# Optimization experiments

Measured on AMD Instinct MI355X. Metric: run time of the kernel, lower is better.

Reference implementation:

```python
import jax, jax.numpy as jnp
import numpy as np

NUM_EXPERTS = 8


def setup_inputs() -> dict:
    key = jax.random.key(0)
    k1, k2, k3, k4, k5 = jax.random.split(key, 5)
    T, D, DFF, E, K = 2048, 2048, 1024, NUM_EXPERTS, 2
    hidden_states = jax.random.normal(k1, (T, D), dtype=jnp.float32)
    w1 = jax.random.normal(k2, (E, 2 * DFF, D), dtype=jnp.float32) * 0.02
    w2 = jax.random.normal(k3, (E, D, DFF), dtype=jnp.float32) * 0.02
    topk_weights = jax.random.uniform(k4, (T, K), dtype=jnp.float32)
    topk_weights = topk_weights / jnp.sum(topk_weights, axis=-1, keepdims=True)
    topk_ids = jax.random.randint(k5, (T, K), 0, E, dtype=jnp.int32)
    return {"hidden_states": hidden_states, "w1": w1, "w2": w2,
            "topk_weights": topk_weights, "topk_ids": topk_ids}


def _expert_fn(x, w1_e, w2_e):
    # x: [T, D], w1_e: [2*DFF, D], w2_e: [D, DFF]
    gu = x @ w1_e.T                      # [T, 2*DFF]
    dff = w2_e.shape[1]
    gate, up = gu[:, :dff], gu[:, dff:]
    h = jax.nn.silu(gate) * up           # SiLU-and-mul activation
    return h @ w2_e.T                    # [T, D]


def reference(hidden_states, w1, w2, topk_weights, topk_ids):
    T = hidden_states.shape[0]
    E = w1.shape[0]
    # route[t, e] = sum_k topk_weights[t,k] * (topk_ids[t,k] == e)
    route = jnp.zeros((T, E), dtype=hidden_states.dtype)
    route = route.at[jnp.arange(T)[:, None], topk_ids].add(topk_weights)
    # per-expert dense GEMMs (E is small and fixed), then weighted combine
    outs = jax.vmap(lambda w1_e, w2_e: _expert_fn(hidden_states, w1_e, w2_e))(w1, w2)  # [E, T, D]
    return jnp.einsum('te,etd->td', route, outs)
```

## Files before the change

### kernel.cpp

```cpp
#include <hip/hip_runtime.h>
#include <hip/hip_bf16.h>
#include <stdint.h>

typedef __attribute__((ext_vector_type(4))) float f32x4;
typedef __attribute__((ext_vector_type(8))) short bf16x8;
typedef unsigned short u16;

#define T_TOK   2048
#define D_DIM   2048
#define DFF_DIM 1024
#define NEXP    8
#define TOPK    2
#define NROWS   (T_TOK * TOPK)
#define BM      128
#define BK      64
#define MAX_MB  40
#define GRID_G  (16 * MAX_MB)

#define XB_OFF    65536
#define XB_BYTES  ((size_t)T_TOK * D_DIM * 2)
#define H_OFF     (XB_OFF + XB_BYTES)
#define H_BYTES   ((size_t)NROWS * DFF_DIM * 2)
#define W1B_OFF   (H_OFF + H_BYTES)
#define W1B_BYTES ((size_t)NEXP * 2 * DFF_DIM * D_DIM * 2)
#define W2B_OFF   (W1B_OFF + W1B_BYTES)
#define W2B_BYTES ((size_t)NEXP * D_DIM * DFF_DIM * 2)
#define WS_NEED   (W2B_OFF + W2B_BYTES)

#define W1_T   ((size_t)NEXP * 2 * DFF_DIM * D_DIM / 8)
#define W2_T   ((size_t)NEXP * D_DIM * DFF_DIM / 8)
#define X_T    ((size_t)T_TOK * D_DIM / 8)
#define PREP_CHUNKS (W1_T + W2_T + X_T)
#define PREP_BLKS 2048

#define PIN() asm volatile("" ::: "memory")
#define BAR_LGKM()                                                        \
    asm volatile("s_waitcnt lgkmcnt(0)" ::: "memory");                    \
    __builtin_amdgcn_s_barrier()

__device__ __forceinline__ u16 f2bf(float f) {
    __hip_bfloat16 h = __float2bfloat16(f);
    return *reinterpret_cast<u16*>(&h);
}

__device__ __forceinline__ void cvt8(const float* src, u16* dst) {
    f32x4 a = *(const f32x4*)src;
    f32x4 b = *(const f32x4*)(src + 4);
    bf16x8 v;
#pragma unroll
    for (int j = 0; j < 4; ++j) { v[j] = (short)f2bf(a[j]); v[j + 4] = (short)f2bf(b[j]); }
    *(bf16x8*)dst = v;
}

__device__ __forceinline__ void cvt8_nt(const float* src, u16* dst) {
    f32x4 a = __builtin_nontemporal_load((const f32x4*)src);
    f32x4 b = __builtin_nontemporal_load(((const f32x4*)src) + 1);
    bf16x8 v;
#pragma unroll
    for (int j = 0; j < 4; ++j) { v[j] = (short)f2bf(a[j]); v[j + 4] = (short)f2bf(b[j]); }
    *(bf16x8*)dst = v;
}

__device__ __forceinline__ void gll16(const u16* gsrc, const u16* lds) {
    __builtin_amdgcn_global_load_lds(
        (const __attribute__((address_space(1))) uint32_t*)gsrc,
        (__attribute__((address_space(3))) uint32_t*)lds, 16, 0, 0);
}

__device__ __forceinline__ bf16x8 lds_read8_swz(const u16* base, int row, int inner) {
    int off = row * 128 + (inner ^ ((row & 7) << 4));
    return *(const bf16x8*)((const char*)base + off);
}

__device__ __forceinline__ void route_body(const int* topk_ids, const float* topk_w,
                                           int* sched, int* row_token, float* row_w,
                                           int* cnt, int* off, int* cur) {
    const int tid = threadIdx.x;
    if (tid < NEXP) cnt[tid] = 0;
    __syncthreads();
    for (int p = tid; p < NROWS; p += blockDim.x)
        atomicAdd(&cnt[topk_ids[p]], 1);
    __syncthreads();
    if (tid == 0) {
        int acc = 0, mb = 0;
        for (int e = 0; e < NEXP; ++e) {
            off[e] = acc;
            int c = cnt[e];
            for (int m0 = 0; m0 < c; m0 += BM) {
                sched[1 + 3 * mb] = e;
                sched[2 + 3 * mb] = acc + m0;
                sched[3 + 3 * mb] = (c - m0 < BM) ? (c - m0) : BM;
                ++mb;
            }
            acc += c;
        }
        sched[0] = mb;
    }
    if (tid < NEXP) cur[tid] = 0;
    __syncthreads();
    for (int p = tid; p < NROWS; p += blockDim.x) {
        int e = topk_ids[p];
        int slot = off[e] + atomicAdd(&cur[e], 1);
        row_token[slot] = p / TOPK;
        row_w[slot]     = topk_w[p];
    }
}

__global__ void prep_kernel(const float* __restrict__ w1, const float* __restrict__ w2,
                            const float* __restrict__ X,
                            u16* __restrict__ w1b, u16* __restrict__ w2b,
                            u16* __restrict__ Xb, float* __restrict__ out,
                            const int* __restrict__ topk_ids,
                            const float* __restrict__ topk_w,
                            int* __restrict__ sched, int* __restrict__ row_token,
                            float* __restrict__ row_w) {
    __shared__ int cnt[NEXP], off[NEXP], cur[NEXP];
    if (blockIdx.x == PREP_BLKS) {
        route_body(topk_ids, topk_w, sched, row_token, row_w, cnt, off, cur);
        return;
    }
    const size_t stride = (size_t)PREP_BLKS * 256;
    for (size_t t = (size_t)blockIdx.x * 256 + threadIdx.x; t < PREP_CHUNKS; t += stride) {
        if (t < W1_T) {
            cvt8_nt(w1 + t * 8, w1b + t * 8);
        } else if (t < W1_T + W2_T) {
            size_t u = t - W1_T;
            cvt8_nt(w2 + u * 8, w2b + u * 8);
        } else {
            size_t u = t - (W1_T + W2_T);
            cvt8_nt(X + u * 8, Xb + u * 8);
            f32x4 z = (f32x4){0.f, 0.f, 0.f, 0.f};
            *(f32x4*)(out + u * 8) = z;
            *(f32x4*)(out + u * 8 + 4) = z;
        }
    }
}

#define DECODE_BLOCK()                                                    \
    const int bid   = blockIdx.x;                                         \
    const int xcd   = bid & 7;                                            \
    const int local = bid >> 3;                                \
    const int n0h   = local / MAX_MB;                          \
    const int mb    = local - n0h * MAX_MB;                               \
    const int n0i   = xcd * 2 + n0h;                           \
    if (mb >= sched[0]) return;                                           \
    const int e    = sched[1 + 3 * mb];                                   \
    const int m0   = sched[2 + 3 * mb];                                   \
    const int mlen = sched[3 + 3 * mb]

#define GLL8(k0)                                                          \
    _Pragma("unroll") for (int i = 0; i < 4; ++i)                         \
        gll16(asrc[i] + (k0), &lA[aoff[i]]);                              \
    _Pragma("unroll") for (int i = 0; i < 4; ++i)                         \
        gll16(bsrc[i] + (k0), &lB[aoff[i]]);

__global__ __launch_bounds__(256, 3)
void gemm1p_kernel(const u16* __restrict__ Xb, const u16* __restrict__ w1b,
                   const int* __restrict__ sched, const int* __restrict__ row_token,
                   u16* __restrict__ H) {
    __shared__ u16 lA[BM * BK];
    __shared__ u16 lB[BM * BK];

    DECODE_BLOCK();
    const int n0 = n0i * 64;

    const int tid  = threadIdx.x;
    const int lane = tid & 63;
    const int wave = tid >> 6;
    const int wm = wave >> 1, wn = wave & 1;
    const int lr = lane & 15, lk = lane >> 4;

    const u16* asrc[4];
    const u16* bsrc[4];
    int aoff[4];
#pragma unroll
    for (int i = 0; i < 4; ++i) {
        int R = i * 32 + wave * 8 + (lane >> 3);
        int grow = m0 + R; if (grow > NROWS - 1) grow = NROWS - 1;
        int tok = row_token[grow];
        int c8 = ((lane & 7) ^ (R & 7)) * 8;
        asrc[i] = Xb + (size_t)tok * D_DIM + c8;
        int gr = (R < 64) ? (n0 + R) : (DFF_DIM + n0 + (R - 64));
        bsrc[i] = w1b + ((size_t)e * (2 * DFF_DIM) + gr) * D_DIM + c8;
        aoff[i] = i * 2048 + wave * 512;
    }

    f32x4 accg[4][2], accu[4][2];
#pragma unroll
    for (int m = 0; m < 4; ++m)
#pragma unroll
        for (int n = 0; n < 2; ++n) {
            accg[m][n] = (f32x4){0.f, 0.f, 0.f, 0.f};
            accu[m][n] = (f32x4){0.f, 0.f, 0.f, 0.f};
        }

    const int KT = D_DIM / BK;
    for (int kt = 0; kt < KT; ++kt) {
        GLL8(kt * BK);
        __syncthreads();
#pragma unroll
        for (int ks = 0; ks < 2; ++ks) {
            const int inner = ks * 64 + lk * 16;
            bf16x8 af[4], bg[2], bu[2];
#pragma unroll
            for (int m = 0; m < 4; ++m)
                af[m] = lds_read8_swz(lA, wm * 64 + m * 16 + lr, inner);
#pragma unroll
            for (int n = 0; n < 2; ++n) {
                bg[n] = lds_read8_swz(lB, wn * 32 + n * 16 + lr, inner);
                bu[n] = lds_read8_swz(lB, 64 + wn * 32 + n * 16 + lr, inner);
            }
#pragma unroll
            for (int m = 0; m < 4; ++m)
#pragma unroll
                for (int n = 0; n < 2; ++n) {
                    accg[m][n] = __builtin_amdgcn_mfma_f32_16x16x32_bf16(af[m], bg[n], accg[m][n], 0, 0, 0);
                    accu[m][n] = __builtin_amdgcn_mfma_f32_16x16x32_bf16(af[m], bu[n], accu[m][n], 0, 0, 0);
                }
        }
        __syncthreads();
    }

#pragma unroll
    for (int m = 0; m < 4; ++m)
#pragma unroll
        for (int n = 0; n < 2; ++n)
#pragma unroll
            for (int r = 0; r < 4; ++r) {
                int rloc = wm * 64 + m * 16 + (lane >> 4) * 4 + r;
                if (rloc < mlen) {
                    int col = wn * 32 + n * 16 + lr;
                    float g = accg[m][n][r], u = accu[m][n][r];
                    float h = (g / (1.f + __expf(-g))) * u;
                    H[(size_t)(m0 + rloc) * DFF_DIM + n0 + col] = f2bf(h);
                }
            }
}

__global__ __launch_bounds__(256, 3)
void gemm2p_kernel(const u16* __restrict__ H, const u16* __restrict__ w2b,
                   const int* __restrict__ sched, const int* __restrict__ row_token,
                   const float* __restrict__ row_w, float* __restrict__ out) {
    __shared__ u16 lA[BM * BK];
    __shared__ u16 lB[BM * BK];

    DECODE_BLOCK();
    const int n0 = n0i * 128;

    const int tid  = threadIdx.x;
    const int lane = tid & 63;
    const int wave = tid >> 6;
    const int wm = wave >> 1, wn = wave & 1;
    const int lr = lane & 15, lk = lane >> 4;

    const u16* asrc[4];
    const u16* bsrc[4];
    int aoff[4];
#pragma unroll
    for (int i = 0; i < 4; ++i) {
        int R = i * 32 + wave * 8 + (lane >> 3);
        int grow = m0 + R; if (grow > NROWS - 1) grow = NROWS - 1;
        int c8 = ((lane & 7) ^ (R & 7)) * 8;
        asrc[i] = H + (size_t)grow * DFF_DIM + c8;
        bsrc[i] = w2b + ((size_t)e * D_DIM + (n0 + R)) * DFF_DIM + c8;
        aoff[i] = i * 2048 + wave * 512;
    }

    f32x4 acc[4][4];
#pragma unroll
    for (int m = 0; m < 4; ++m)
#pragma unroll
        for (int n = 0; n < 4; ++n) acc[m][n] = (f32x4){0.f, 0.f, 0.f, 0.f};

    const int KT = DFF_DIM / BK;
    for (int kt = 0; kt < KT; ++kt) {
        GLL8(kt * BK);
        __syncthreads();
#pragma unroll
        for (int ks = 0; ks < 2; ++ks) {
            const int inner = ks * 64 + lk * 16;
            bf16x8 af[4], bfr[4];
#pragma unroll
            for (int m = 0; m < 4; ++m)
                af[m] = lds_read8_swz(lA, wm * 64 + m * 16 + lr, inner);
#pragma unroll
            for (int n = 0; n < 4; ++n)
                bfr[n] = lds_read8_swz(lB, wn * 64 + n * 16 + lr, inner);
#pragma unroll
            for (int m = 0; m < 4; ++m)
#pragma unroll
                for (int n = 0; n < 4; ++n)
                    acc[m][n] = __builtin_amdgcn_mfma_f32_16x16x32_bf16(af[m], bfr[n], acc[m][n], 0, 0, 0);
        }
        __syncthreads();
    }

#pragma unroll
    for (int m = 0; m < 4; ++m)
#pragma unroll
        for (int n = 0; n < 4; ++n)
#pragma unroll
            for (int r = 0; r < 4; ++r) {
                int rloc = wm * 64 + m * 16 + (lane >> 4) * 4 + r;
                if (rloc < mlen) {
                    int grow = m0 + rloc;
                    int tok  = row_token[grow];
                    float w  = row_w[grow];
                    int col  = wn * 64 + n * 16 + lr;
                    atomicAdd(&out[(size_t)tok * D_DIM + n0 + col], acc[m][n][r] * w);
                }
            }
}

__global__ void cvt_x_kernel(const float* __restrict__ X, u16* __restrict__ Xb,
                             float* __restrict__ out) {
    int idx = (blockIdx.x * 256 + threadIdx.x) * 8;
    cvt8(X + idx, Xb + idx);
    f32x4 z = (f32x4){0.f, 0.f, 0.f, 0.f};
    *(f32x4*)(out + idx) = z;
    *(f32x4*)(out + idx + 4) = z;
}

__global__ void route_kernel(const int* __restrict__ topk_ids,
                             const float* __restrict__ topk_w,
                             int* __restrict__ sched,
                             int* __restrict__ row_token,
                             float* __restrict__ row_w) {
    __shared__ int cnt[NEXP], off[NEXP], cur[NEXP];
    route_body(topk_ids, topk_w, sched, row_token, row_w, cnt, off, cur);
}

#define GLL_A(k0, dst)                                                    \
    _Pragma("unroll") for (int i = 0; i < 4; ++i)                         \
        gll16(asrc[i] + (k0), &(dst)[aoff[i]]);

#define LOAD_RB(rb, k0)                                                   \
    _Pragma("unroll") for (int i = 0; i < 4; ++i) {                       \
        rb[i][0] = *(const f32x4*)(bptr[i] + (k0));                       \
        rb[i][1] = *(const f32x4*)(bptr[i] + (k0) + 4);                   \
    }

#define CVT_WRITE(rb, dst)                                                \
    _Pragma("unroll") for (int i = 0; i < 4; ++i) {                       \
        bf16x8 vb;                                                        \
        _Pragma("unroll") for (int j = 0; j < 4; ++j) {                   \
            vb[j] = (short)f2bf(rb[i][0][j]);                             \
            vb[j + 4] = (short)f2bf(rb[i][1][j]);                         \
        }                                                                 \
        *(bf16x8*)((char*)(dst) + wroff[i]) = vb;                         \
    }

__global__ __launch_bounds__(256, 3)
void gemm1f_kernel(const u16* __restrict__ Xb, const float* __restrict__ w1,
                   const int* __restrict__ sched, const int* __restrict__ row_token,
                   u16* __restrict__ H) {
    __shared__ u16 lA[2][BM * BK];
    __shared__ u16 lB[BM * BK];

    DECODE_BLOCK();
    const int n0 = n0i * 64;

    const int tid  = threadIdx.x;
    const int lane = tid & 63;
    const int wave = tid >> 6;
    const int wm = wave >> 1, wn = wave & 1;
    const int lr = lane & 15, lk = lane >> 4;

    const u16* asrc[4];
    int aoff[4];
#pragma unroll
    for (int i = 0; i < 4; ++i) {
        int R = i * 32 + wave * 8 + (lane >> 3);
        int grow = m0 + R; if (grow > NROWS - 1) grow = NROWS - 1;
        int tok = row_token[grow];
        asrc[i] = Xb + (size_t)tok * D_DIM + (size_t)(((lane & 7) ^ (R & 7)) * 8);
        aoff[i] = i * 2048 + wave * 512;
    }
    const float* bptr[4];
    int wroff[4];
#pragma unroll
    for (int i = 0; i < 4; ++i) {
        int chunk = i * 256 + tid;
        int row = chunk >> 3, c8 = chunk & 7;
        int gcol = (row < 64) ? (n0 + row) : (DFF_DIM + n0 + (row - 64));
        bptr[i] = w1 + ((size_t)e * (2 * DFF_DIM) + gcol) * D_DIM + c8 * 8;
        wroff[i] = row * 128 + ((c8 * 16) ^ ((row & 7) << 4));
    }

    f32x4 rb[4][2];
    f32x4 accg[4][2], accu[4][2];
#pragma unroll
    for (int m = 0; m < 4; ++m)
#pragma unroll
        for (int n = 0; n < 2; ++n) {
            accg[m][n] = (f32x4){0.f, 0.f, 0.f, 0.f};
            accu[m][n] = (f32x4){0.f, 0.f, 0.f, 0.f};
        }

#define MFMA_G1(bufA, bufB)                                               \
    _Pragma("unroll") for (int ks = 0; ks < 2; ++ks) {                    \
        const int inner = ks * 64 + lk * 16;                              \
        bf16x8 af[4], bg[2], bu[2];                                       \
        _Pragma("unroll") for (int m = 0; m < 4; ++m)                     \
            af[m] = lds_read8_swz(bufA, wm * 64 + m * 16 + lr, inner);    \
        _Pragma("unroll") for (int n = 0; n < 2; ++n) {                   \
            bg[n] = lds_read8_swz(bufB, wn * 32 + n * 16 + lr, inner);    \
            bu[n] = lds_read8_swz(bufB, 64 + wn * 32 + n * 16 + lr, inner); \
        }                                                                 \
        _Pragma("unroll") for (int m = 0; m < 4; ++m)                     \
            _Pragma("unroll") for (int n = 0; n < 2; ++n) {               \
                accg[m][n] = __builtin_amdgcn_mfma_f32_16x16x32_bf16(af[m], bg[n], accg[m][n], 0, 0, 0); \
                accu[m][n] = __builtin_amdgcn_mfma_f32_16x16x32_bf16(af[m], bu[n], accu[m][n], 0, 0, 0); \
            }                                                             \
    }

    const int KT = D_DIM / BK;
    LOAD_RB(rb, 0);
    GLL_A(0, lA[0]);
    CVT_WRITE(rb, lB);
    __syncthreads();

    for (int kt = 0, cur = 0; kt < KT; ++kt, cur ^= 1) {
        if (kt + 1 < KT) {
            LOAD_RB(rb, (kt + 1) * BK);
            GLL_A((kt + 1) * BK, lA[cur ^ 1]);
        }
        PIN();
        MFMA_G1(lA[cur], lB);
        BAR_LGKM();
        if (kt + 1 < KT) { CVT_WRITE(rb, lB); }
        __syncthreads();
    }
#undef MFMA_G1

#pragma unroll
    for (int m = 0; m < 4; ++m)
#pragma unroll
        for (int n = 0; n < 2; ++n)
#pragma unroll
            for (int r = 0; r < 4; ++r) {
                int rloc = wm * 64 + m * 16 + (lane >> 4) * 4 + r;
                if (rloc < mlen) {
                    int col = wn * 32 + n * 16 + lr;
                    float g = accg[m][n][r], u = accu[m][n][r];
                    float h = (g / (1.f + __expf(-g))) * u;
                    H[(size_t)(m0 + rloc) * DFF_DIM + n0 + col] = f2bf(h);
                }
            }
}

__global__ __launch_bounds__(256, 3)
void gemm2f_kernel(const u16* __restrict__ H, const float* __restrict__ w2,
                   const int* __restrict__ sched, const int* __restrict__ row_token,
                   const float* __restrict__ row_w, float* __restrict__ out) {
    __shared__ u16 lA[2][BM * BK];
    __shared__ u16 lB[BM * BK];

    DECODE_BLOCK();
    const int n0 = n0i * 128;

    const int tid  = threadIdx.x;
    const int lane = tid & 63;
    const int wave = tid >> 6;
    const int wm = wave >> 1, wn = wave & 1;
    const int lr = lane & 15, lk = lane >> 4;

    const u16* asrc[4];
    int aoff[4];
#pragma unroll
    for (int i = 0; i < 4; ++i) {
        int R = i * 32 + wave * 8 + (lane >> 3);
        int grow = m0 + R; if (grow > NROWS - 1) grow = NROWS - 1;
        asrc[i] = H + (size_t)grow * DFF_DIM + (size_t)(((lane & 7) ^ (R & 7)) * 8);
        aoff[i] = i * 2048 + wave * 512;
    }
    const float* bptr[4];
    int wroff[4];
#pragma unroll
    for (int i = 0; i < 4; ++i) {
        int chunk = i * 256 + tid;
        int row = chunk >> 3, c8 = chunk & 7;
        bptr[i] = w2 + ((size_t)e * D_DIM + (n0 + row)) * DFF_DIM + c8 * 8;
        wroff[i] = row * 128 + ((c8 * 16) ^ ((row & 7) << 4));
    }

    f32x4 rb[4][2];
    f32x4 acc[4][4];
#pragma unroll
    for (int m = 0; m < 4; ++m)
#pragma unroll
        for (int n = 0; n < 4; ++n) acc[m][n] = (f32x4){0.f, 0.f, 0.f, 0.f};

#define MFMA_G2(bufA, bufB)                                               \
    _Pragma("unroll") for (int ks = 0; ks < 2; ++ks) {                    \
        const int inner = ks * 64 + lk * 16;                              \
        bf16x8 af[4], bfr[4];                                             \
        _Pragma("unroll") for (int m = 0; m < 4; ++m)                     \
            af[m] = lds_read8_swz(bufA, wm * 64 + m * 16 + lr, inner);    \
        _Pragma("unroll") for (int n = 0; n < 4; ++n)                     \
            bfr[n] = lds_read8_swz(bufB, wn * 64 + n * 16 + lr, inner);   \
        _Pragma("unroll") for (int m = 0; m < 4; ++m)                     \
            _Pragma("unroll") for (int n = 0; n < 4; ++n)                 \
                acc[m][n] = __builtin_amdgcn_mfma_f32_16x16x32_bf16(af[m], bfr[n], acc[m][n], 0, 0, 0); \
    }

    const int KT = DFF_DIM / BK;
    LOAD_RB(rb, 0);
    GLL_A(0, lA[0]);
    CVT_WRITE(rb, lB);
    __syncthreads();

    for (int kt = 0, cur = 0; kt < KT; ++kt, cur ^= 1) {
        if (kt + 1 < KT) {
            LOAD_RB(rb, (kt + 1) * BK);
            GLL_A((kt + 1) * BK, lA[cur ^ 1]);
        }
        PIN();
        MFMA_G2(lA[cur], lB);
        BAR_LGKM();
        if (kt + 1 < KT) { CVT_WRITE(rb, lB); }
        __syncthreads();
    }
#undef MFMA_G2

#pragma unroll
    for (int m = 0; m < 4; ++m)
#pragma unroll
        for (int n = 0; n < 4; ++n)
#pragma unroll
            for (int r = 0; r < 4; ++r) {
                int rloc = wm * 64 + m * 16 + (lane >> 4) * 4 + r;
                if (rloc < mlen) {
                    int grow = m0 + rloc;
                    int tok  = row_token[grow];
                    float w  = row_w[grow];
                    int col  = wn * 64 + n * 16 + lr;
                    atomicAdd(&out[(size_t)tok * D_DIM + n0 + col], acc[m][n][r] * w);
                }
            }
}

extern "C" void kernel_launch(void* const* d_in, const int* in_sizes, int n_in,
                              void* d_out, int out_size, void* d_ws, size_t ws_size,
                              hipStream_t stream) {
    const float* X  = (const float*)d_in[0];
    const float* w1 = (const float*)d_in[1];
    const float* w2 = (const float*)d_in[2];
    const float* tw = (const float*)d_in[3];
    const int*   ti = (const int*)d_in[4];

    int*   sched     = (int*)d_ws;
    int*   row_token = (int*)((char*)d_ws + 512);
    float* row_w     = (float*)((char*)d_ws + 512 + 4 * NROWS);
    u16*   Xb        = (u16*)((char*)d_ws + XB_OFF);
    u16*   H         = (u16*)((char*)d_ws + H_OFF);

    if (ws_size >= WS_NEED) {
        u16* w1b = (u16*)((char*)d_ws + W1B_OFF);
        u16* w2b = (u16*)((char*)d_ws + W2B_OFF);
        prep_kernel<<<PREP_BLKS + 1, 256, 0, stream>>>(w1, w2, X, w1b, w2b, Xb,
                                                       (float*)d_out, ti, tw,
                                                       sched, row_token, row_w);
        gemm1p_kernel<<<GRID_G, 256, 0, stream>>>(Xb, w1b, sched, row_token, H);
        gemm2p_kernel<<<GRID_G, 256, 0, stream>>>(H, w2b, sched, row_token, row_w, (float*)d_out);
    } else {
        route_kernel<<<1, 256, 0, stream>>>(ti, tw, sched, row_token, row_w);
        cvt_x_kernel<<<(T_TOK * D_DIM) / (256 * 8), 256, 0, stream>>>(X, Xb, (float*)d_out);
        gemm1f_kernel<<<GRID_G, 256, 0, stream>>>(Xb, w1, sched, row_token, H);
        gemm2f_kernel<<<GRID_G, 256, 0, stream>>>(H, w2, sched, row_token, row_w, (float*)d_out);
    }
}
```

Baseline: 166.7 us.

## Overlap w2 bf16 conversion with first GEMM by appending conversion blocks

The fp32-to-bf16 conversion of w2 is taken out of the prep kernel and done by 256 extra blocks appended to the first expert GEMM launch. The w2 conversion is not needed until the second GEMM, so it can run alongside GEMM1 instead of delaying it in the prep kernel. The trade-off is that these memory-bound blocks compete with GEMM1 blocks for bandwidth and CU slots, and they run at the tail of the grid, which could lengthen GEMM1.

```diff
diff --git a/kernel.cpp b/kernel.cpp
--- a/kernel.cpp
+++ b/kernel.cpp
@@ -16,6 +16,7 @@
 #define BK      64
 #define MAX_MB  40
 #define GRID_G  (16 * MAX_MB)
+#define CVT2_BLKS 256
 
 #define XB_OFF    65536
 #define XB_BYTES  ((size_t)T_TOK * D_DIM * 2)
@@ -30,7 +31,7 @@
 #define W1_T   ((size_t)NEXP * 2 * DFF_DIM * D_DIM / 8)
 #define W2_T   ((size_t)NEXP * D_DIM * DFF_DIM / 8)
 #define X_T    ((size_t)T_TOK * D_DIM / 8)
-#define PREP_CHUNKS (W1_T + W2_T + X_T)
+#define PREP_CHUNKS_A (W1_T + X_T)
 #define PREP_BLKS 2048
 
 #define PIN() asm volatile("" ::: "memory")
@@ -106,10 +107,9 @@
     }
 }
 
-__global__ void prep_kernel(const float* __restrict__ w1, const float* __restrict__ w2,
-                            const float* __restrict__ X,
-                            u16* __restrict__ w1b, u16* __restrict__ w2b,
-                            u16* __restrict__ Xb, float* __restrict__ out,
+__global__ void prep_kernel(const float* __restrict__ w1, const float* __restrict__ X,
+                            u16* __restrict__ w1b, u16* __restrict__ Xb,
+                            float* __restrict__ out,
                             const int* __restrict__ topk_ids,
                             const float* __restrict__ topk_w,
                             int* __restrict__ sched, int* __restrict__ row_token,
@@ -120,14 +120,11 @@
         return;
     }
     const size_t stride = (size_t)PREP_BLKS * 256;
-    for (size_t t = (size_t)blockIdx.x * 256 + threadIdx.x; t < PREP_CHUNKS; t += stride) {
+    for (size_t t = (size_t)blockIdx.x * 256 + threadIdx.x; t < PREP_CHUNKS_A; t += stride) {
         if (t < W1_T) {
             cvt8_nt(w1 + t * 8, w1b + t * 8);
-        } else if (t < W1_T + W2_T) {
+        } else {
             size_t u = t - W1_T;
-            cvt8_nt(w2 + u * 8, w2b + u * 8);
-        } else {
-            size_t u = t - (W1_T + W2_T);
             cvt8_nt(X + u * 8, Xb + u * 8);
             f32x4 z = (f32x4){0.f, 0.f, 0.f, 0.f};
             *(f32x4*)(out + u * 8) = z;
@@ -157,9 +154,18 @@
 __global__ __launch_bounds__(256, 3)
 void gemm1p_kernel(const u16* __restrict__ Xb, const u16* __restrict__ w1b,
                    const int* __restrict__ sched, const int* __restrict__ row_token,
-                   u16* __restrict__ H) {
+                   u16* __restrict__ H,
+                   const float* __restrict__ w2f, u16* __restrict__ w2b) {
     __shared__ u16 lA[BM * BK];
     __shared__ u16 lB[BM * BK];
+
+    if (blockIdx.x >= GRID_G) {
+        const size_t stride = (size_t)CVT2_BLKS * 256;
+        for (size_t t = (size_t)(blockIdx.x - GRID_G) * 256 + threadIdx.x;
+             t < W2_T; t += stride)
+            cvt8_nt(w2f + t * 8, w2b + t * 8);
+        return;
+    }
 
     DECODE_BLOCK();
     const int n0 = n0i * 64;
@@ -558,10 +564,11 @@
     if (ws_size >= WS_NEED) {
         u16* w1b = (u16*)((char*)d_ws + W1B_OFF);
         u16* w2b = (u16*)((char*)d_ws + W2B_OFF);
-        prep_kernel<<<PREP_BLKS + 1, 256, 0, stream>>>(w1, w2, X, w1b, w2b, Xb,
+        prep_kernel<<<PREP_BLKS + 1, 256, 0, stream>>>(w1, X, w1b, Xb,
                                                        (float*)d_out, ti, tw,
                                                        sched, row_token, row_w);
-        gemm1p_kernel<<<GRID_G, 256, 0, stream>>>(Xb, w1b, sched, row_token, H);
+        gemm1p_kernel<<<GRID_G + CVT2_BLKS, 256, 0, stream>>>(Xb, w1b, sched, row_token, H,
+                                                              w2, w2b);
         gemm2p_kernel<<<GRID_G, 256, 0, stream>>>(H, w2b, sched, row_token, row_w, (float*)d_out);
     } else {
         route_kernel<<<1, 256, 0, stream>>>(ti, tw, sched, row_token, row_w);
```

Result: no change. 164.1 us (-1.5%).
